# Kernel tuning notes

Hardware: AMD Instinct MI355X
Metric: run time of the kernel (lower is better)

Reference implementation:

```python
import jax, jax.numpy as jnp
import numpy as np
from jax import lax

B, S, V, E, H, T = 64, 256, 50000, 300, 256, 13  # H = hidden per direction (512//2)


def setup_inputs() -> dict:
    key = jax.random.key(0)
    ks = iter(jax.random.split(key, 48))
    def rn(shape, s=0.05):
        return jax.random.normal(next(ks), shape, jnp.float32) * s
    inp = {}
    inp["x"] = jax.random.randint(next(ks), (B, S), 0, V)
    inp["pos"] = jax.random.normal(next(ks), (B, S), jnp.float32)
    inp["emb"] = rn((V, E), 1.0)
    # LSTM layer 0 (input E=300), layer 1 (input 2H=512); [dir, 4H, in]/[dir,4H,H]/[dir,4H]
    inp["lstm_Wih0"] = rn((2, 4 * H, E))
    inp["lstm_Whh0"] = rn((2, 4 * H, H))
    inp["lstm_b0"] = rn((2, 4 * H))
    inp["lstm_Wih1"] = rn((2, 4 * H, 2 * H))
    inp["lstm_Whh1"] = rn((2, 4 * H, H))
    inp["lstm_b1"] = rn((2, 4 * H))
    # PositionFeedForward (dim_model = hidden = S = 256)
    inp["pos_fc1_w"] = rn((S, S)); inp["pos_fc1_b"] = rn((S,))
    inp["pos_fc2_w"] = rn((S, S)); inp["pos_fc2_b"] = rn((S,))
    inp["pos_ln_g"] = jnp.ones((S,)); inp["pos_ln_b"] = jnp.zeros((S,))
    # conditionLinear: hidden_size(512) -> pad_size(256), stored [in,out]
    inp["cond_w"] = rn((2 * H, S)); inp["cond_b"] = rn((S,))
    # ConditionalLayerNorm(pad_size)
    inp["cln_weight"] = jnp.ones((S,)); inp["cln_bias"] = jnp.zeros((S,))
    inp["cln_wd"] = rn((S, S)); inp["cln_bd"] = rn((S, S))
    # SelfAttention(pad_size) on the [B,S] sentence vector
    inp["att_wq"] = rn((S, S)); inp["att_bq"] = rn((S,))
    inp["att_wk"] = rn((S, S)); inp["att_bk"] = rn((S,))
    inp["att_wv"] = rn((S, S)); inp["att_bv"] = rn((S,))
    inp["att_ln_g"] = jnp.ones((S,)); inp["att_ln_b"] = jnp.zeros((S,))
    # attLinear: pad_size -> 1
    inp["attlin_w"] = rn((S, 1)); inp["attlin_b"] = rn((1,))
    # final linear: pad_size -> tag_num
    inp["out_w"] = rn((S, T)); inp["out_b"] = rn((T,))
    # CRF params
    inp["crf_start"] = rn((T,), 0.1)
    inp["crf_end"] = rn((T,), 0.1)
    inp["crf_trans"] = rn((T, T), 0.1)
    return inp


def _layer_norm(x, g, b, eps=1e-5):
    m = jnp.mean(x, -1, keepdims=True)
    v = jnp.mean((x - m) ** 2, -1, keepdims=True)
    return (x - m) / jnp.sqrt(v + eps) * g + b


def _lstm_dir(x, Wih, Whh, b, reverse):
    # x: [B,S,in] -> hs [B,S,H]; PyTorch gate order i,f,g,o
    xt = jnp.swapaxes(x, 0, 1)  # [S,B,in]
    xg = jnp.einsum('sbi,gi->sbg', xt, Wih) + b  # precompute input gates [S,B,4H]
    def step(carry, g_in):
        h, c = carry
        g = g_in + h @ Whh.T
        i, f, gg, o = jnp.split(g, 4, axis=-1)
        c = jax.nn.sigmoid(f) * c + jax.nn.sigmoid(i) * jnp.tanh(gg)
        h = jax.nn.sigmoid(o) * jnp.tanh(c)
        return (h, c), h
    init = (jnp.zeros((x.shape[0], H), x.dtype), jnp.zeros((x.shape[0], H), x.dtype))
    _, hs = lax.scan(step, init, xg, reverse=reverse)
    return jnp.swapaxes(hs, 0, 1)


def _bilstm_layer(x, Wih, Whh, b):
    fwd = _lstm_dir(x, Wih[0], Whh[0], b[0], False)
    bwd = _lstm_dir(x, Wih[1], Whh[1], b[1], True)
    return jnp.concatenate([fwd, bwd], axis=-1)


def _viterbi(em, start, end, trans):
    # em: [B,S,T] -> best tag path [B,S] (full-length mask, as in torchcrf decode)
    score0 = start + em[:, 0]  # [B,T]
    def step(score, em_t):
        nxt = score[:, :, None] + trans[None] + em_t[:, None, :]  # [B,T,T]
        return jnp.max(nxt, axis=1), jnp.argmax(nxt, axis=1)
    score, hist = lax.scan(step, score0, jnp.swapaxes(em[:, 1:], 0, 1))  # hist [S-1,B,T]
    last = jnp.argmax(score + end, axis=-1)  # [B]
    def back(tag, idx_t):
        prev = jnp.take_along_axis(idx_t, tag[:, None], axis=1)[:, 0]
        return prev, prev
    _, tags_rev = lax.scan(back, last, hist, reverse=True)  # [S-1,B]
    tags = jnp.concatenate([tags_rev, last[None]], axis=0)  # [S,B]
    return jnp.swapaxes(tags, 0, 1)


def reference(x, pos, emb, lstm_Wih0, lstm_Whh0, lstm_b0, lstm_Wih1, lstm_Whh1, lstm_b1,
              pos_fc1_w, pos_fc1_b, pos_fc2_w, pos_fc2_b, pos_ln_g, pos_ln_b,
              cond_w, cond_b, cln_weight, cln_bias, cln_wd, cln_bd,
              att_wq, att_bq, att_wk, att_bk, att_wv, att_bv, att_ln_g, att_ln_b,
              attlin_w, attlin_b, out_w, out_b, crf_start, crf_end, crf_trans):
    out = emb[x]  # [B,S,E]
    out = _bilstm_layer(out, lstm_Wih0, lstm_Whh0, lstm_b0)  # [B,S,2H]
    out = _bilstm_layer(out, lstm_Wih1, lstm_Whh1, lstm_b1)  # [B,S,2H]
    # PositionFeedForward on pos [B,S]
    h = jax.nn.relu(pos @ pos_fc1_w + pos_fc1_b) @ pos_fc2_w + pos_fc2_b
    pos_out = _layer_norm(h + pos, pos_ln_g, pos_ln_b)
    # conditionLinear: [B,S,2H] -> [B,S,S]
    out = out @ cond_w + cond_b
    # ConditionalLayerNorm with cond=pos_out, eps=1e-12
    cond = pos_out[:, None, :]  # [B,1,S]
    w = cond @ cln_wd.T + cln_weight  # weight_dense is Linear(no bias): c @ W.T; stored square, use .T
    bb = cond @ cln_bd.T + cln_bias
    mean = jnp.mean(out, -1, keepdims=True)
    cen = out - mean
    var = jnp.mean(cen ** 2, -1, keepdims=True)
    out = cen / jnp.sqrt(var + 1e-12) * w + bb
    # sentence attention over [B,S]
    sentence = (out @ attlin_w + attlin_b)[..., 0]  # [B,S]
    Q = sentence @ att_wq + att_bq
    K = sentence @ att_wk + att_bk
    Vv = sentence @ att_wv + att_bv
    alpha = jax.nn.softmax(Q * K / jnp.sqrt(jnp.float32(S)), axis=-1)
    att = _layer_norm(alpha * Vv, att_ln_g, att_ln_b)  # [B,S]
    out = out * att[:, :, None]
    logits = out @ out_w + out_b  # [B,S,T]
    tag = _viterbi(logits, crf_start, crf_end, crf_trans)
    return (logits, tag)
```

## Files before the change

kernel.cpp:

```cpp
#include <hip/hip_runtime.h>
#include <math.h>

#define B_    64
#define S_    256
#define E_    300
#define H_    256
#define T_    13
#define G4_   1024
#define D2H_  512

typedef short bf16x8 __attribute__((ext_vector_type(8)));
typedef float f32x4  __attribute__((ext_vector_type(4)));
typedef unsigned int u32x4 __attribute__((ext_vector_type(4)));
typedef unsigned short u16;
typedef unsigned int   u32;
typedef unsigned long long u64;

#define SENT32 0x7F7F7F7Fu

__device__ __forceinline__ float sigf(float x)   { return __builtin_amdgcn_rcpf(1.f + __expf(-x)); }
__device__ __forceinline__ float tanhf_(float x) { return __builtin_amdgcn_rcpf(1.f + __expf(-2.f*x))*2.f - 1.f; }

__device__ __forceinline__ u16 f2bf(float f) {
  union { float f; unsigned u; } v; v.f = f;
  unsigned r = v.u + 0x7fff + ((v.u >> 16) & 1);
  return (u16)(r >> 16);
}
__device__ __forceinline__ float bf2f(u16 h) {
  union { unsigned u; float f; } v; v.u = ((unsigned)h) << 16;
  return v.f;
}

__device__ __forceinline__ u64 cload64(const u64* p) {
  return __hip_atomic_load(p, __ATOMIC_RELAXED, __HIP_MEMORY_SCOPE_AGENT);
}
__device__ __forceinline__ void cstore32(u32* p, u32 v) {
  __hip_atomic_store(p, v, __ATOMIC_RELAXED, __HIP_MEMORY_SCOPE_AGENT);
}

__global__ __launch_bounds__(64)
void k_embed(const int* __restrict__ x, const float* __restrict__ emb,
             u16* __restrict__ oh, u16* __restrict__ ol) {
  int bs = blockIdx.x;
  int xv = x[bs];
  const float4* src = (const float4*)(emb + (size_t)xv * E_);
  u64* dh = (u64*)(oh + (size_t)bs * 320);
  u64* dl = (u64*)(ol + (size_t)bs * 320);
  for (int q = threadIdx.x; q < 80; q += 64) {
    float4 v = (q < 75) ? src[q] : make_float4(0.f, 0.f, 0.f, 0.f);
    u16 hh[4], ll[4];
    float vv[4] = {v.x, v.y, v.z, v.w};
    #pragma unroll
    for (int j = 0; j < 4; j++) {
      hh[j] = f2bf(vv[j]);
      ll[j] = f2bf(vv[j] - bf2f(hh[j]));
    }
    dh[q] = (u64)hh[0] | ((u64)hh[1] << 16) | ((u64)hh[2] << 32) | ((u64)hh[3] << 48);
    dl[q] = (u64)ll[0] | ((u64)ll[1] << 16) | ((u64)ll[2] << 32) | ((u64)ll[3] << 48);
  }
}

__global__ __launch_bounds__(256)
void k_cvtbf2(const float* __restrict__ w, u16* __restrict__ hi, u16* __restrict__ lo, int n) {
  int i = blockIdx.x * 256 + threadIdx.x;
  if (i < n) {
    float v = w[i];
    u16 h = f2bf(v);
    hi[i] = h;
    lo[i] = f2bf(v - bf2f(h));
  }
}

__global__ __launch_bounds__(256)
void k_cvtpad(const float* __restrict__ w, u16* __restrict__ hi, u16* __restrict__ lo,
              int Ksrc, int Kpad, int perm) {
  int r = blockIdx.x;
  int rl = r & 1023, dd = r >> 10;
  int ro = perm ? ((dd << 10) | ((rl & 255) << 2) | (rl >> 8)) : r;
  for (int k = threadIdx.x; k < Kpad; k += 256) {
    float v = (k < Ksrc) ? w[(size_t)r * Ksrc + k] : 0.f;
    u16 h = f2bf(v);
    hi[(size_t)ro * Kpad + k] = h;
    lo[(size_t)ro * Kpad + k] = f2bf(v - bf2f(h));
  }
}

__global__ __launch_bounds__(256)
void k_permb(const float* __restrict__ b, float* __restrict__ bp) {
  int i = blockIdx.x * 256 + threadIdx.x;
  int rl = i & 1023, dd = i >> 10;
  bp[(dd << 10) | ((rl & 255) << 2) | (rl >> 8)] = b[i];
}

__global__ __launch_bounds__(256)
void k_cvtT(const float* __restrict__ w, u16* __restrict__ hi, u16* __restrict__ lo) {
  int n = blockIdx.x;
  for (int k = threadIdx.x; k < 512; k += 256) {
    float v = w[(size_t)k * 256 + n];
    u16 h = f2bf(v);
    hi[(size_t)n * 512 + k] = h;
    lo[(size_t)n * 512 + k] = f2bf(v - bf2f(h));
  }
}

__global__ __launch_bounds__(256)
void k_bgemm(const u16* __restrict__ Ahi, const u16* __restrict__ Alo,
             const u16* __restrict__ Whi, const u16* __restrict__ Wlo,
             const float* __restrict__ bias, float* __restrict__ C,
             int K, int N, int permute, long wStride, long bStride, long cStride)
{
  __shared__ u16 Ash[2][128 * 40];
  __shared__ u16 Wsh[2][128 * 40];

  int tid = threadIdx.x;
  int d   = blockIdx.z;
  int n0  = blockIdx.x * 128, m0 = blockIdx.y * 128;
  int lane = tid & 63;
  int w    = tid >> 6;
  int l15  = lane & 15;
  int quad = lane >> 4;
  int mh = (w >> 1) * 64, nh = (w & 1) * 64;

  int comp = tid >> 7, row = tid & 127;
  int gr = m0 + row;
  int ar = permute ? ((gr & 63) * S_ + (gr >> 6)) : gr;
  const u16* Asrc = (comp ? Alo : Ahi) + (size_t)ar * K;
  const u16* Wsrc = (comp ? Wlo : Whi) + (size_t)d * wStride + (size_t)(n0 + row) * K;
  u16* AshC = &Ash[comp][row * 40];
  u16* WshC = &Wsh[comp][row * 40];

  f32x4 acc[4][4];
  #pragma unroll
  for (int mt = 0; mt < 4; mt++)
    #pragma unroll
    for (int nt = 0; nt < 4; nt++) acc[mt][nt] = (f32x4)(0.f);

  float4 a0 = *(const float4*)(Asrc);
  float4 a1 = *(const float4*)(Asrc + 8);
  float4 a2 = *(const float4*)(Asrc + 16);
  float4 a3 = *(const float4*)(Asrc + 24);
  float4 w0 = *(const float4*)(Wsrc);
  float4 w1 = *(const float4*)(Wsrc + 8);
  float4 w2 = *(const float4*)(Wsrc + 16);
  float4 w3 = *(const float4*)(Wsrc + 24);

  for (int k0 = 0; k0 < K; k0 += 32) {
    __syncthreads();
    *(float4*)(AshC)      = a0; *(float4*)(AshC + 8)  = a1;
    *(float4*)(AshC + 16) = a2; *(float4*)(AshC + 24) = a3;
    *(float4*)(WshC)      = w0; *(float4*)(WshC + 8)  = w1;
    *(float4*)(WshC + 16) = w2; *(float4*)(WshC + 24) = w3;
    __syncthreads();

    if (k0 + 32 < K) {
      a0 = *(const float4*)(Asrc + k0 + 32);
      a1 = *(const float4*)(Asrc + k0 + 40);
      a2 = *(const float4*)(Asrc + k0 + 48);
      a3 = *(const float4*)(Asrc + k0 + 56);
      w0 = *(const float4*)(Wsrc + k0 + 32);
      w1 = *(const float4*)(Wsrc + k0 + 40);
      w2 = *(const float4*)(Wsrc + k0 + 48);
      w3 = *(const float4*)(Wsrc + k0 + 56);
    }

    bf16x8 ah[4], al[4], bh[4], bl[4];
    #pragma unroll
    for (int mt = 0; mt < 4; mt++) {
      int rr = mh + mt * 16 + l15;
      ah[mt] = *(const bf16x8*)&Ash[0][rr * 40 + quad * 8];
      al[mt] = *(const bf16x8*)&Ash[1][rr * 40 + quad * 8];
    }
    #pragma unroll
    for (int nt = 0; nt < 4; nt++) {
      int rr = nh + nt * 16 + l15;
      bh[nt] = *(const bf16x8*)&Wsh[0][rr * 40 + quad * 8];
      bl[nt] = *(const bf16x8*)&Wsh[1][rr * 40 + quad * 8];
    }
    #pragma unroll
    for (int mt = 0; mt < 4; mt++)
      #pragma unroll
      for (int nt = 0; nt < 4; nt++) {
        acc[mt][nt] = __builtin_amdgcn_mfma_f32_16x16x32_bf16(ah[mt], bh[nt], acc[mt][nt], 0, 0, 0);
        acc[mt][nt] = __builtin_amdgcn_mfma_f32_16x16x32_bf16(ah[mt], bl[nt], acc[mt][nt], 0, 0, 0);
        acc[mt][nt] = __builtin_amdgcn_mfma_f32_16x16x32_bf16(al[mt], bh[nt], acc[mt][nt], 0, 0, 0);
      }
  }

  const float* biasd = bias + (size_t)d * bStride;
  float* Cd = C + (size_t)d * cStride;
  #pragma unroll
  for (int nt = 0; nt < 4; nt++) {
    int cn = n0 + nh + nt * 16 + l15;
    float bv = biasd[cn];
    #pragma unroll
    for (int mt = 0; mt < 4; mt++) {
      int mr = m0 + mh + mt * 16 + quad * 4;
      #pragma unroll
      for (int j = 0; j < 4; j++)
        Cd[(size_t)(mr + j) * N + cn] = acc[mt][nt][j] + bv;
    }
  }
}

__global__ __launch_bounds__(256, 1)
void k_lstm_mfma(const float* __restrict__ xg,
                 const u16* __restrict__ Whi, const u16* __restrict__ Wlo,
                 u16* __restrict__ houth, u16* __restrict__ houtl,
                 u32* __restrict__ hbx)
{
  __shared__ __align__(16) u16 hsh[4 * 256];
  __shared__ __align__(16) u16 hsl[4 * 256];

  int tid  = threadIdx.x;
  int us   = blockIdx.x & 7;
  int bg   = (blockIdx.x >> 3) & 15;
  int d    = blockIdx.x >> 7;
  int lane = tid & 63;
  int w    = tid >> 6;
  int l15  = lane & 15;
  int quad = lane >> 4;
  int bpc  = l15 & 3;

  bf16x8 afh[2][8], afl[2][8];
  {
    const u16* WbH = Whi + ((size_t)d * G4_ + (size_t)(l15 & 3) * 256
                            + us * 32 + w * 8 + (l15 >> 2)) * H_;
    const u16* WbL = Wlo + ((size_t)d * G4_ + (size_t)(l15 & 3) * 256
                            + us * 32 + w * 8 + (l15 >> 2)) * H_;
    #pragma unroll
    for (int mt = 0; mt < 2; mt++)
      #pragma unroll
      for (int kt = 0; kt < 8; kt++) {
        afh[mt][kt] = *(const bf16x8*)(WbH + (size_t)mt * 4 * H_ + kt * 32 + quad * 8);
        afl[mt][kt] = *(const bf16x8*)(WbL + (size_t)mt * 4 * H_ + kt * 32 + quad * 8);
      }
  }

  float c0 = 0.f, c1 = 0.f;
  u32 pk0 = 0, pk1 = 0;

  int pb  = tid >> 6;
  int pu0 = (tid & 63) << 2;
  bool mine = (pu0 >> 5) == us;
  int pwoff = ((pb * 256 + pu0) * 2) ^ ((pb & 1) << 6);

  int u0c   = us * 32 + w * 8 + quad;
  int soff0 = ((bpc * 256 + u0c) * 2)     ^ ((bpc & 1) << 6);
  int soff1 = ((bpc * 256 + u0c + 4) * 2) ^ ((bpc & 1) << 6);

  const float* xgd = xg + (size_t)d * S_ * B_ * G4_;
  u32* hb = hbx + (size_t)(d * 16 + bg) * S_ * 1024;

  for (int it = 0; it < S_; it++) {
    int s = d ? (S_ - 1 - it) : it;

    f32x4 accA[2], accB[2];
    const float* xgrow = xgd + ((size_t)s * B_ + (bg * 4 + bpc)) * G4_
                       + (size_t)(us * 32 + w * 8 + quad) * 4;
    accA[0] = *(const f32x4*)(xgrow);
    accA[1] = *(const f32x4*)(xgrow + 16);
    accB[0] = (f32x4)(0.f);
    accB[1] = (f32x4)(0.f);

    if (it > 0) {
      if (!mine) {
        const u64* src = (const u64*)(hb + (size_t)(it - 1) * 1024 + pb * 256 + pu0);
        u64 a = cload64(src), b2 = cload64(src + 1);
        while (((u32)a == SENT32) | ((u32)(a >> 32) == SENT32) |
               ((u32)b2 == SENT32) | ((u32)(b2 >> 32) == SENT32)) {
          __builtin_amdgcn_s_sleep(1);
          a = cload64(src); b2 = cload64(src + 1);
        }
        u64 hi64 = (a & 0xFFFFull) | (((a >> 32) & 0xFFFFull) << 16)
                 | ((b2 & 0xFFFFull) << 32) | (((b2 >> 32) & 0xFFFFull) << 48);
        u64 lo64 = ((a >> 16) & 0xFFFFull) | (((a >> 48) & 0xFFFFull) << 16)
                 | (((b2 >> 16) & 0xFFFFull) << 32) | ((b2 >> 48) << 48);
        *(u64*)((char*)hsh + pwoff) = hi64;
        *(u64*)((char*)hsl + pwoff) = lo64;
      }
      if (l15 < 4) {
        *(u16*)((char*)hsh + soff0) = (u16)pk0;
        *(u16*)((char*)hsl + soff0) = (u16)(pk0 >> 16);
        *(u16*)((char*)hsh + soff1) = (u16)pk1;
        *(u16*)((char*)hsl + soff1) = (u16)(pk1 >> 16);
      }
      __syncthreads();

      #pragma unroll
      for (int kt = 0; kt < 8; kt++) {
        int coff = ((bpc * 256 + (kt * 4 + quad) * 8) * 2) ^ ((bpc & 1) << 6);
        bf16x8 bh = *(const bf16x8*)((const char*)hsh + coff);
        bf16x8 bl = *(const bf16x8*)((const char*)hsl + coff);
        #pragma unroll
        for (int mt = 0; mt < 2; mt++) {
          accA[mt] = __builtin_amdgcn_mfma_f32_16x16x32_bf16(afh[mt][kt], bh, accA[mt], 0, 0, 0);
          accB[mt] = __builtin_amdgcn_mfma_f32_16x16x32_bf16(afh[mt][kt], bl, accB[mt], 0, 0, 0);
          accB[mt] = __builtin_amdgcn_mfma_f32_16x16x32_bf16(afl[mt][kt], bh, accB[mt], 0, 0, 0);
        }
      }
    }

    u32* hbrow = hb + (size_t)it * 1024 + bpc * 256 + u0c;
    {
      f32x4 g0 = accA[0] + accB[0];
      c0 = sigf(g0[1]) * c0 + sigf(g0[0]) * tanhf_(g0[2]);
      float h0 = sigf(g0[3]) * tanhf_(c0);
      u16 hh = f2bf(h0), hl = f2bf(h0 - bf2f(hh));
      pk0 = (u32)hh | ((u32)hl << 16);
      if (l15 < 4) cstore32(hbrow, pk0);
    }
    {
      f32x4 g1 = accA[1] + accB[1];
      c1 = sigf(g1[1]) * c1 + sigf(g1[0]) * tanhf_(g1[2]);
      float h1 = sigf(g1[3]) * tanhf_(c1);
      u16 hh = f2bf(h1), hl = f2bf(h1 - bf2f(hh));
      pk1 = (u32)hh | ((u32)hl << 16);
      if (l15 < 4) cstore32(hbrow + 4, pk1);
    }

    {
      u32 x1_0 = __shfl(pk0, l15 + 16), x1_1 = __shfl(pk1, l15 + 16);
      u32 x2_0 = __shfl(pk0, l15 + 32), x2_1 = __shfl(pk1, l15 + 32);
      u32 x3_0 = __shfl(pk0, l15 + 48), x3_1 = __shfl(pk1, l15 + 48);
      if (lane < 4) {
        u32x4 hivec, lovec;
        hivec[0] = (pk0 & 0xFFFFu)  | ((x1_0 & 0xFFFFu) << 16);
        hivec[1] = (x2_0 & 0xFFFFu) | ((x3_0 & 0xFFFFu) << 16);
        hivec[2] = (pk1 & 0xFFFFu)  | ((x1_1 & 0xFFFFu) << 16);
        hivec[3] = (x2_1 & 0xFFFFu) | ((x3_1 & 0xFFFFu) << 16);
        lovec[0] = (pk0 >> 16)  | (x1_0 & 0xFFFF0000u);
        lovec[1] = (x2_0 >> 16) | (x3_0 & 0xFFFF0000u);
        lovec[2] = (pk1 >> 16)  | (x1_1 & 0xFFFF0000u);
        lovec[3] = (x2_1 >> 16) | (x3_1 & 0xFFFF0000u);
        size_t ho = ((size_t)(bg * 4 + lane) * S_ + s) * D2H_ + d * H_ + us * 32 + w * 8;
        *(u32x4*)(houth + ho) = hivec;
        *(u32x4*)(houtl + ho) = lovec;
      }
    }

    __syncthreads();
  }
}

__device__ __forceinline__ float bsum(float v, float* sb) {
  int t = threadIdx.x;
  sb[t] = v; __syncthreads();
  for (int s = 128; s; s >>= 1) { if (t < s) sb[t] += sb[t + s]; __syncthreads(); }
  float r = sb[0]; __syncthreads(); return r;
}
__device__ __forceinline__ float bmax(float v, float* sb) {
  int t = threadIdx.x;
  sb[t] = v; __syncthreads();
  for (int s = 128; s; s >>= 1) { if (t < s) sb[t] = fmaxf(sb[t], sb[t + s]); __syncthreads(); }
  float r = sb[0]; __syncthreads(); return r;
}

__global__ __launch_bounds__(256)
void k_pos(const float* __restrict__ pos, const float* __restrict__ fc1w, const float* __restrict__ fc1b,
           const float* __restrict__ fc2w, const float* __restrict__ fc2b,
           const float* __restrict__ lng, const float* __restrict__ lnb, float* __restrict__ pos_out)
{
  __shared__ float sp[256], sh[256], sb[256];
  int b = blockIdx.x, t = threadIdx.x;
  sp[t] = pos[b * 256 + t];
  __syncthreads();
  float a1 = fc1b[t];
  for (int s = 0; s < 256; s++) a1 += sp[s] * fc1w[s * 256 + t];
  a1 = fmaxf(a1, 0.f);
  sh[t] = a1; __syncthreads();
  float a2 = fc2b[t] + sp[t];
  for (int s = 0; s < 256; s++) a2 += sh[s] * fc2w[s * 256 + t];
  float m   = bsum(a2, sb) * (1.f / 256.f);
  float cen = a2 - m;
  float var = bsum(cen * cen, sb) * (1.f / 256.f);
  pos_out[b * 256 + t] = cen * rsqrtf(var + 1e-5f) * lng[t] + lnb[t];
}

__global__ __launch_bounds__(256)
void k_clnA(const float* __restrict__ pos_out, const float* __restrict__ wd, const float* __restrict__ bd,
            const float* __restrict__ cw, const float* __restrict__ cb,
            float* __restrict__ wvec, float* __restrict__ bbvec)
{
  __shared__ float sp[256];
  int b = blockIdx.x, t = threadIdx.x;
  sp[t] = pos_out[b * 256 + t];
  __syncthreads();
  const float4* wdr = (const float4*)(wd + (size_t)t * 256);
  const float4* bdr = (const float4*)(bd + (size_t)t * 256);
  float aw = 0.f, ab = 0.f;
  for (int q = 0; q < 64; q++) {
    float4 w4 = wdr[q], b4 = bdr[q];
    float s0 = sp[q*4], s1 = sp[q*4+1], s2 = sp[q*4+2], s3 = sp[q*4+3];
    aw += s0*w4.x + s1*w4.y + s2*w4.z + s3*w4.w;
    ab += s0*b4.x + s1*b4.y + s2*b4.z + s3*b4.w;
  }
  wvec [b * 256 + t] = aw + cw[t];
  bbvec[b * 256 + t] = ab + cb[t];
}

__global__ __launch_bounds__(256)
void k_clnB(const float* __restrict__ oc, const float* __restrict__ wvec, const float* __restrict__ bbvec,
            const float* __restrict__ alw, const float* __restrict__ alb,
            float* __restrict__ outn, float* __restrict__ sentence)
{
  __shared__ float sb[256];
  int bs = blockIdx.x, t = threadIdx.x;
  int b = bs >> 8;
  float v   = oc[(size_t)bs * 256 + t];
  float m   = bsum(v, sb) * (1.f / 256.f);
  float cen = v - m;
  float var = bsum(cen * cen, sb) * (1.f / 256.f);
  float o   = cen * rsqrtf(var + 1e-12f) * wvec[b * 256 + t] + bbvec[b * 256 + t];
  outn[(size_t)bs * 256 + t] = o;
  float sv = bsum(o * alw[t], sb);
  if (t == 0) sentence[bs] = sv + alb[0];
}

__global__ __launch_bounds__(256)
void k_att(const float* __restrict__ sentence,
           const float* __restrict__ wq, const float* __restrict__ bq,
           const float* __restrict__ wk, const float* __restrict__ bk,
           const float* __restrict__ wv, const float* __restrict__ bv,
           const float* __restrict__ lng, const float* __restrict__ lnb,
           float* __restrict__ att)
{
  __shared__ float ss[256], sb[256];
  int b = blockIdx.x, t = threadIdx.x;
  ss[t] = sentence[b * 256 + t];
  __syncthreads();
  float q = bq[t], k = bk[t], vv = bv[t];
  for (int s = 0; s < 256; s++) {
    float sv = ss[s];
    q  += sv * wq[s * 256 + t];
    k  += sv * wk[s * 256 + t];
    vv += sv * wv[s * 256 + t];
  }
  float x  = q * k * (1.f / 16.f);
  float mx = bmax(x, sb);
  float e  = expf(x - mx);
  float sm = bsum(e, sb);
  float a  = (e / sm) * vv;
  float m   = bsum(a, sb) * (1.f / 256.f);
  float cen = a - m;
  float var = bsum(cen * cen, sb) * (1.f / 256.f);
  att[b * 256 + t] = cen * rsqrtf(var + 1e-5f) * lng[t] + lnb[t];
}

__global__ __launch_bounds__(64)
void k_out(const float* __restrict__ outn, const float* __restrict__ att,
           const float* __restrict__ ow, const float* __restrict__ ob,
           float* __restrict__ logits)
{
  __shared__ float row[256];
  int bs = blockIdx.x, t = threadIdx.x;
  ((float4*)row)[t] = ((const float4*)(outn + (size_t)bs * 256))[t];
  __syncthreads();
  float a = att[bs];
  if (t < T_) {
    float acc = 0.f;
    for (int c = 0; c < 256; c++) acc += row[c] * ow[c * T_ + t];
    logits[(size_t)bs * T_ + t] = a * acc + ob[t];
  }
}

__global__ __launch_bounds__(64)
void k_viterbi(const float* __restrict__ logits, const float* __restrict__ start,
               const float* __restrict__ endv, const float* __restrict__ trans,
               float* __restrict__ tags)
{
  __shared__ float sc[16];
  __shared__ float str[169];
  __shared__ unsigned char hist[255 * 13];
  __shared__ int tg[256];
  int b = blockIdx.x, t = threadIdx.x;
  for (int i = t; i < 169; i += 64) str[i] = trans[i];
  if (t < 13) sc[t] = start[t] + logits[((size_t)b * 256) * 13 + t];
  __syncthreads();
  for (int s = 1; s < 256; s++) {
    float best = -1e30f; int bi = 0;
    if (t < 13) {
      best = sc[0] + str[t]; bi = 0;
      for (int i = 1; i < 13; i++) {
        float v = sc[i] + str[i * 13 + t];
        if (v > best) { best = v; bi = i; }
      }
    }
    __syncthreads();
    if (t < 13) {
      sc[t] = best + logits[((size_t)b * 256 + s) * 13 + t];
      hist[(s - 1) * 13 + t] = (unsigned char)bi;
    }
    __syncthreads();
  }
  if (t == 0) {
    float best = sc[0] + endv[0]; int last = 0;
    for (int j = 1; j < 13; j++) {
      float v = sc[j] + endv[j];
      if (v > best) { best = v; last = j; }
    }
    tg[255] = last;
    int cur = last;
    for (int s = 254; s >= 0; s--) { cur = hist[s * 13 + cur]; tg[s] = cur; }
  }
  __syncthreads();
  for (int s = t; s < 256; s += 64) tags[b * 256 + s] = (float)tg[s];
}

extern "C" void kernel_launch(void* const* d_in, const int* in_sizes, int n_in,
                              void* d_out, int out_size, void* d_ws, size_t ws_size,
                              hipStream_t stream)
{
  const int*   x     = (const int*)  d_in[0];
  const float* pos   = (const float*)d_in[1];
  const float* emb   = (const float*)d_in[2];
  const float* Wih0  = (const float*)d_in[3];
  const float* Whh0  = (const float*)d_in[4];
  const float* b0    = (const float*)d_in[5];
  const float* Wih1  = (const float*)d_in[6];
  const float* Whh1  = (const float*)d_in[7];
  const float* b1    = (const float*)d_in[8];
  const float* fc1w  = (const float*)d_in[9];
  const float* fc1b  = (const float*)d_in[10];
  const float* fc2w  = (const float*)d_in[11];
  const float* fc2b  = (const float*)d_in[12];
  const float* plng  = (const float*)d_in[13];
  const float* plnb  = (const float*)d_in[14];
  const float* condw = (const float*)d_in[15];
  const float* condb = (const float*)d_in[16];
  const float* clnw  = (const float*)d_in[17];
  const float* clnb  = (const float*)d_in[18];
  const float* clnwd = (const float*)d_in[19];
  const float* clnbd = (const float*)d_in[20];
  const float* wq    = (const float*)d_in[21];
  const float* bq    = (const float*)d_in[22];
  const float* wk    = (const float*)d_in[23];
  const float* bk    = (const float*)d_in[24];
  const float* wv    = (const float*)d_in[25];
  const float* bv    = (const float*)d_in[26];
  const float* atlng = (const float*)d_in[27];
  const float* atlnb = (const float*)d_in[28];
  const float* alw   = (const float*)d_in[29];
  const float* alb   = (const float*)d_in[30];
  const float* ow    = (const float*)d_in[31];
  const float* ob    = (const float*)d_in[32];
  const float* cstart= (const float*)d_in[33];
  const float* cend  = (const float*)d_in[34];
  const float* ctrans= (const float*)d_in[35];

  const size_t BS = (size_t)B_ * S_;
  float* ws = (float*)d_ws;
  float* r1   = ws;
  float* xg   = r1 + 5242880;
  float* l0r  = xg + 33554432;
  float* l1r  = l0r + 8388608;
  float* pos_out  = l1r + 8388608;
  float* wvec     = pos_out + 16384;
  float* bbvec    = wvec + 16384;
  float* sentence = bbvec + 16384;
  float* attv     = sentence + 16384;
  unsigned* flags = (unsigned*)(attv + 16384);
  u16* whhh0 = (u16*)(flags + 65536);
  u16* whhl0 = whhh0 + 524288;
  u16* whhh1 = whhl0 + 524288;
  u16* whhl1 = whhh1 + 524288;
  u16* wih0h = whhl1 + 524288;
  u16* wih0l = wih0h + 655360;
  u16* wih1h = wih0l + 655360;
  u16* wih1l = wih1h + 1048576;
  u16* condTh = wih1l + 1048576;
  u16* condTl = condTh + 131072;
  float* b0p  = (float*)(condTl + 131072);
  float* b1p  = b0p + 2048;

  u16* embh = (u16*)r1;
  u16* embl = embh + 5242880;
  float* out_cond = r1;
  u16* l0h = (u16*)l0r;
  u16* l0l = l0h + 8388608;
  u16* l1h = (u16*)l1r;
  u16* l1l = l1h + 8388608;
  u32* hb0 = (u32*)l1r;
  u32* hb1 = (u32*)l0r;
  const size_t HBBYTES = (size_t)32 * S_ * 1024 * sizeof(u32);
  float* outn = l0r;
  float* logits = (float*)d_out;
  float* tags   = logits + BS * T_;

  hipMemsetAsync(hb0, 0x7F, HBBYTES, stream);

  k_embed <<<dim3(B_ * S_), dim3(64), 0, stream>>>(x, emb, embh, embl);
  k_cvtbf2<<<dim3(2048), dim3(256), 0, stream>>>(Whh0, whhh0, whhl0, 2 * G4_ * H_);
  k_cvtbf2<<<dim3(2048), dim3(256), 0, stream>>>(Whh1, whhh1, whhl1, 2 * G4_ * H_);
  k_cvtpad<<<dim3(2048), dim3(256), 0, stream>>>(Wih0, wih0h, wih0l, 300, 320, 1);
  k_cvtpad<<<dim3(2048), dim3(256), 0, stream>>>(Wih1, wih1h, wih1l, 512, 512, 1);
  k_permb <<<dim3(8),    dim3(256), 0, stream>>>(b0, b0p);
  k_permb <<<dim3(8),    dim3(256), 0, stream>>>(b1, b1p);
  k_cvtT  <<<dim3(256),  dim3(256), 0, stream>>>(condw, condTh, condTl);

  k_bgemm<<<dim3(8, 128, 2), dim3(256), 0, stream>>>(
      embh, embl, wih0h, wih0l, b0p, xg, 320, G4_, 1,
      (long)G4_ * 320, (long)G4_, (long)BS * G4_);
  k_lstm_mfma<<<dim3(256), dim3(256), 0, stream>>>(
      xg, whhh0, whhl0, l0h, l0l, hb0);

  k_bgemm<<<dim3(8, 128, 2), dim3(256), 0, stream>>>(
      l0h, l0l, wih1h, wih1l, b1p, xg, 512, G4_, 1,
      (long)G4_ * 512, (long)G4_, (long)BS * G4_);
  hipMemsetAsync(hb1, 0x7F, HBBYTES, stream);
  k_lstm_mfma<<<dim3(256), dim3(256), 0, stream>>>(
      xg, whhh1, whhl1, l1h, l1l, hb1);

  k_bgemm<<<dim3(2, 128, 1), dim3(256), 0, stream>>>(
      l1h, l1l, condTh, condTl, condb, out_cond, 512, 256, 0, 0, 0, 0);

  k_pos <<<dim3(B_), dim3(256), 0, stream>>>(pos, fc1w, fc1b, fc2w, fc2b, plng, plnb, pos_out);
  k_clnA<<<dim3(B_), dim3(256), 0, stream>>>(pos_out, clnwd, clnbd, clnw, clnb, wvec, bbvec);
  k_clnB<<<dim3(B_ * S_), dim3(256), 0, stream>>>(out_cond, wvec, bbvec, alw, alb, outn, sentence);
  k_att <<<dim3(B_), dim3(256), 0, stream>>>(sentence, wq, bq, wk, bk, wv, bv, atlng, atlnb, attv);
  k_out <<<dim3(B_ * S_), dim3(64), 0, stream>>>(outn, attv, ow, ob, logits);
  k_viterbi<<<dim3(B_), dim3(64), 0, stream>>>(logits, cstart, cend, ctrans, tags);
}
```

Baseline: 1.538 ms.

## Double-buffer LSTM hidden-state LDS, merge weight-prep and pos/cln kernels

The recurrent LSTM kernel now keeps two LDS buffers for the hidden state, alternating per timestep, so the trailing __syncthreads at the end of each step can be dropped. This halves the block barriers on the serial 256-step critical path. The seven weight-conversion and bias-permute launches become a single k_prep launch, and k_pos plus k_clnA become one k_poscln kernel. Fewer launches and no pos_out round trip through global memory, at the cost of branchy prep blocks.

```diff
diff --git a/kernel.cpp b/kernel.cpp
--- a/kernel.cpp
+++ b/kernel.cpp
@@ -61,45 +61,63 @@
 }
 
 __global__ __launch_bounds__(256)
-void k_cvtbf2(const float* __restrict__ w, u16* __restrict__ hi, u16* __restrict__ lo, int n) {
-  int i = blockIdx.x * 256 + threadIdx.x;
-  if (i < n) {
-    float v = w[i];
+void k_prep(const float* __restrict__ Whh0, const float* __restrict__ Whh1,
+            u16* __restrict__ whhh0, u16* __restrict__ whhl0,
+            u16* __restrict__ whhh1, u16* __restrict__ whhl1,
+            const float* __restrict__ Wih0, const float* __restrict__ Wih1,
+            u16* __restrict__ wih0h, u16* __restrict__ wih0l,
+            u16* __restrict__ wih1h, u16* __restrict__ wih1l,
+            const float* __restrict__ b0, const float* __restrict__ b1,
+            float* __restrict__ b0p, float* __restrict__ b1p,
+            const float* __restrict__ condw,
+            u16* __restrict__ condTh, u16* __restrict__ condTl)
+{
+  int bid = blockIdx.x, t = threadIdx.x;
+  if (bid < 2048) {
+    int i = bid * 256 + t;
+    float v = Whh0[i];
     u16 h = f2bf(v);
-    hi[i] = h;
-    lo[i] = f2bf(v - bf2f(h));
-  }
-}
-
-__global__ __launch_bounds__(256)
-void k_cvtpad(const float* __restrict__ w, u16* __restrict__ hi, u16* __restrict__ lo,
-              int Ksrc, int Kpad, int perm) {
-  int r = blockIdx.x;
-  int rl = r & 1023, dd = r >> 10;
-  int ro = perm ? ((dd << 10) | ((rl & 255) << 2) | (rl >> 8)) : r;
-  for (int k = threadIdx.x; k < Kpad; k += 256) {
-    float v = (k < Ksrc) ? w[(size_t)r * Ksrc + k] : 0.f;
+    whhh0[i] = h; whhl0[i] = f2bf(v - bf2f(h));
+  } else if (bid < 4096) {
+    int i = (bid - 2048) * 256 + t;
+    float v = Whh1[i];
     u16 h = f2bf(v);
-    hi[(size_t)ro * Kpad + k] = h;
-    lo[(size_t)ro * Kpad + k] = f2bf(v - bf2f(h));
-  }
-}
-
-__global__ __launch_bounds__(256)
-void k_permb(const float* __restrict__ b, float* __restrict__ bp) {
-  int i = blockIdx.x * 256 + threadIdx.x;
-  int rl = i & 1023, dd = i >> 10;
-  bp[(dd << 10) | ((rl & 255) << 2) | (rl >> 8)] = b[i];
-}
-
-__global__ __launch_bounds__(256)
-void k_cvtT(const float* __restrict__ w, u16* __restrict__ hi, u16* __restrict__ lo) {
-  int n = blockIdx.x;
-  for (int k = threadIdx.x; k < 512; k += 256) {
-    float v = w[(size_t)k * 256 + n];
-    u16 h = f2bf(v);
-    hi[(size_t)n * 512 + k] = h;
-    lo[(size_t)n * 512 + k] = f2bf(v - bf2f(h));
+    whhh1[i] = h; whhl1[i] = f2bf(v - bf2f(h));
+  } else if (bid < 6144) {
+    int r = bid - 4096;
+    int rl = r & 1023, dd = r >> 10;
+    int ro = (dd << 10) | ((rl & 255) << 2) | (rl >> 8);
+    for (int k = t; k < 320; k += 256) {
+      float v = (k < 300) ? Wih0[(size_t)r * 300 + k] : 0.f;
+      u16 h = f2bf(v);
+      wih0h[(size_t)ro * 320 + k] = h;
+      wih0l[(size_t)ro * 320 + k] = f2bf(v - bf2f(h));
+    }
+  } else if (bid < 8192) {
+    int r = bid - 6144;
+    int rl = r & 1023, dd = r >> 10;
+    int ro = (dd << 10) | ((rl & 255) << 2) | (rl >> 8);
+    for (int k = t; k < 512; k += 256) {
+      float v = Wih1[(size_t)r * 512 + k];
+      u16 h = f2bf(v);
+      wih1h[(size_t)ro * 512 + k] = h;
+      wih1l[(size_t)ro * 512 + k] = f2bf(v - bf2f(h));
+    }
+  } else if (bid < 8448) {
+    int n = bid - 8192;
+    for (int k = t; k < 512; k += 256) {
+      float v = condw[(size_t)k * 256 + n];
+      u16 h = f2bf(v);
+      condTh[(size_t)n * 512 + k] = h;
+      condTl[(size_t)n * 512 + k] = f2bf(v - bf2f(h));
+    }
+  } else {
+    for (int i = t; i < 2048; i += 256) {
+      int rl = i & 1023, dd = i >> 10;
+      int o = (dd << 10) | ((rl & 255) << 2) | (rl >> 8);
+      b0p[o] = b0[i];
+      b1p[o] = b1[i];
+    }
   }
 }
 
@@ -208,8 +226,8 @@
                  u16* __restrict__ houth, u16* __restrict__ houtl,
                  u32* __restrict__ hbx)
 {
-  __shared__ __align__(16) u16 hsh[4 * 256];
-  __shared__ __align__(16) u16 hsl[4 * 256];
+  __shared__ __align__(16) u16 hsh[2][1024];
+  __shared__ __align__(16) u16 hsl[2][1024];
 
   int tid  = threadIdx.x;
   int us   = blockIdx.x & 7;
@@ -263,6 +281,9 @@
     accB[1] = (f32x4)(0.f);
 
     if (it > 0) {
+      int p = (it - 1) & 1;
+      char* shp = (char*)hsh[p];
+      char* slp = (char*)hsl[p];
       if (!mine) {
         const u64* src = (const u64*)(hb + (size_t)(it - 1) * 1024 + pb * 256 + pu0);
         u64 a = cload64(src), b2 = cload64(src + 1);
@@ -275,22 +296,22 @@
                  | ((b2 & 0xFFFFull) << 32) | (((b2 >> 32) & 0xFFFFull) << 48);
         u64 lo64 = ((a >> 16) & 0xFFFFull) | (((a >> 48) & 0xFFFFull) << 16)
                  | (((b2 >> 16) & 0xFFFFull) << 32) | ((b2 >> 48) << 48);
-        *(u64*)((char*)hsh + pwoff) = hi64;
-        *(u64*)((char*)hsl + pwoff) = lo64;
+        *(u64*)(shp + pwoff) = hi64;
+        *(u64*)(slp + pwoff) = lo64;
       }
       if (l15 < 4) {
-        *(u16*)((char*)hsh + soff0) = (u16)pk0;
-        *(u16*)((char*)hsl + soff0) = (u16)(pk0 >> 16);
-        *(u16*)((char*)hsh + soff1) = (u16)pk1;
-        *(u16*)((char*)hsl + soff1) = (u16)(pk1 >> 16);
+        *(u16*)(shp + soff0) = (u16)pk0;
+        *(u16*)(slp + soff0) = (u16)(pk0 >> 16);
+        *(u16*)(shp + soff1) = (u16)pk1;
+        *(u16*)(slp + soff1) = (u16)(pk1 >> 16);
       }
       __syncthreads();
 
       #pragma unroll
       for (int kt = 0; kt < 8; kt++) {
         int coff = ((bpc * 256 + (kt * 4 + quad) * 8) * 2) ^ ((bpc & 1) << 6);
-        bf16x8 bh = *(const bf16x8*)((const char*)hsh + coff);
-        bf16x8 bl = *(const bf16x8*)((const char*)hsl + coff);
+        bf16x8 bh = *(const bf16x8*)((const char*)shp + coff);
+        bf16x8 bl = *(const bf16x8*)((const char*)slp + coff);
         #pragma unroll
         for (int mt = 0; mt < 2; mt++) {
           accA[mt] = __builtin_amdgcn_mfma_f32_16x16x32_bf16(afh[mt][kt], bh, accA[mt], 0, 0, 0);
@@ -337,8 +358,6 @@
         *(u32x4*)(houtl + ho) = lovec;
       }
     }
-
-    __syncthreads();
   }
 }
 
@@ -356,11 +375,14 @@
 }
 
 __global__ __launch_bounds__(256)
-void k_pos(const float* __restrict__ pos, const float* __restrict__ fc1w, const float* __restrict__ fc1b,
-           const float* __restrict__ fc2w, const float* __restrict__ fc2b,
-           const float* __restrict__ lng, const float* __restrict__ lnb, float* __restrict__ pos_out)
-{
-  __shared__ float sp[256], sh[256], sb[256];
+void k_poscln(const float* __restrict__ pos, const float* __restrict__ fc1w, const float* __restrict__ fc1b,
+              const float* __restrict__ fc2w, const float* __restrict__ fc2b,
+              const float* __restrict__ lng, const float* __restrict__ lnb,
+              const float* __restrict__ wd, const float* __restrict__ bd,
+              const float* __restrict__ cw, const float* __restrict__ cb,
+              float* __restrict__ wvec, float* __restrict__ bbvec)
+{
+  __shared__ float sp[256], sh[256], sb[256], spo[256];
   int b = blockIdx.x, t = threadIdx.x;
   sp[t] = pos[b * 256 + t];
   __syncthreads();
@@ -373,24 +395,14 @@
   float m   = bsum(a2, sb) * (1.f / 256.f);
   float cen = a2 - m;
   float var = bsum(cen * cen, sb) * (1.f / 256.f);
-  pos_out[b * 256 + t] = cen * rsqrtf(var + 1e-5f) * lng[t] + lnb[t];
-}
-
-__global__ __launch_bounds__(256)
-void k_clnA(const float* __restrict__ pos_out, const float* __restrict__ wd, const float* __restrict__ bd,
-            const float* __restrict__ cw, const float* __restrict__ cb,
-            float* __restrict__ wvec, float* __restrict__ bbvec)
-{
-  __shared__ float sp[256];
-  int b = blockIdx.x, t = threadIdx.x;
-  sp[t] = pos_out[b * 256 + t];
+  spo[t] = cen * rsqrtf(var + 1e-5f) * lng[t] + lnb[t];
   __syncthreads();
   const float4* wdr = (const float4*)(wd + (size_t)t * 256);
   const float4* bdr = (const float4*)(bd + (size_t)t * 256);
   float aw = 0.f, ab = 0.f;
   for (int q = 0; q < 64; q++) {
     float4 w4 = wdr[q], b4 = bdr[q];
-    float s0 = sp[q*4], s1 = sp[q*4+1], s2 = sp[q*4+2], s3 = sp[q*4+3];
+    float s0 = spo[q*4], s1 = spo[q*4+1], s2 = spo[q*4+2], s3 = spo[q*4+3];
     aw += s0*w4.x + s1*w4.y + s2*w4.z + s3*w4.w;
     ab += s0*b4.x + s1*b4.y + s2*b4.z + s3*b4.w;
   }
@@ -589,13 +601,10 @@
   hipMemsetAsync(hb0, 0x7F, HBBYTES, stream);
 
   k_embed <<<dim3(B_ * S_), dim3(64), 0, stream>>>(x, emb, embh, embl);
-  k_cvtbf2<<<dim3(2048), dim3(256), 0, stream>>>(Whh0, whhh0, whhl0, 2 * G4_ * H_);
-  k_cvtbf2<<<dim3(2048), dim3(256), 0, stream>>>(Whh1, whhh1, whhl1, 2 * G4_ * H_);
-  k_cvtpad<<<dim3(2048), dim3(256), 0, stream>>>(Wih0, wih0h, wih0l, 300, 320, 1);
-  k_cvtpad<<<dim3(2048), dim3(256), 0, stream>>>(Wih1, wih1h, wih1l, 512, 512, 1);
-  k_permb <<<dim3(8),    dim3(256), 0, stream>>>(b0, b0p);
-  k_permb <<<dim3(8),    dim3(256), 0, stream>>>(b1, b1p);
-  k_cvtT  <<<dim3(256),  dim3(256), 0, stream>>>(condw, condTh, condTl);
+  k_prep  <<<dim3(8449), dim3(256), 0, stream>>>(
+      Whh0, Whh1, whhh0, whhl0, whhh1, whhl1,
+      Wih0, Wih1, wih0h, wih0l, wih1h, wih1l,
+      b0, b1, b0p, b1p, condw, condTh, condTl);
 
   k_bgemm<<<dim3(8, 128, 2), dim3(256), 0, stream>>>(
       embh, embl, wih0h, wih0l, b0p, xg, 320, G4_, 1,
@@ -613,8 +622,8 @@
   k_bgemm<<<dim3(2, 128, 1), dim3(256), 0, stream>>>(
       l1h, l1l, condTh, condTl, condb, out_cond, 512, 256, 0, 0, 0, 0);
 
-  k_pos <<<dim3(B_), dim3(256), 0, stream>>>(pos, fc1w, fc1b, fc2w, fc2b, plng, plnb, pos_out);
-  k_clnA<<<dim3(B_), dim3(256), 0, stream>>>(pos_out, clnwd, clnbd, clnw, clnb, wvec, bbvec);
+  k_poscln<<<dim3(B_), dim3(256), 0, stream>>>(
+      pos, fc1w, fc1b, fc2w, fc2b, plng, plnb, clnwd, clnbd, clnw, clnb, wvec, bbvec);
   k_clnB<<<dim3(B_ * S_), dim3(256), 0, stream>>>(out_cond, wvec, bbvec, alw, alb, outn, sentence);
   k_att <<<dim3(B_), dim3(256), 0, stream>>>(sentence, wq, bq, wk, bk, wv, bv, atlng, atlnb, attv);
   k_out <<<dim3(B_ * S_), dim3(64), 0, stream>>>(outn, attv, ow, ob, logits);
```

Result: no change. 1.545 ms (+0.5%).
